# Kernel tuning notes

Hardware: AMD Instinct MI355X
Metric: run time of the kernel (lower is better)

Reference implementation:

```python
import jax, jax.numpy as jnp
import numpy as np

K = 20          # neighbors, hardcoded default in source
EPS = 1e-5      # BatchNorm2d default eps


def _knn(x, k=K):
    # x: (B, C, N). distance[b,i,j] = -||x_i - x_j||^2; top-k == first k of descending sort
    inner = -2.0 * jnp.einsum('bdn,bdm->bnm', x, x)
    xx = jnp.sum(x * x, axis=1)                      # (B, N)
    dist = -xx[:, :, None] - inner - xx[:, None, :]  # (B, N, N)
    return jax.lax.top_k(dist, k)[1]                 # (B, N, k) int32


def _graph_feature(x, k=K):
    idx = _knn(x, k)
    xt = jnp.transpose(x, (0, 2, 1))                 # (B, N, C)
    feat = jax.vmap(lambda a, i: a[i])(xt, idx)      # (B, N, k, C) gather
    center = jnp.broadcast_to(xt[:, :, None, :], feat.shape)
    out = jnp.concatenate([feat - center, center], axis=-1)  # (B, N, k, 2C)
    return jnp.transpose(out, (0, 3, 1, 2))          # (B, 2C, N, k)


def _conv_bn_relu(x, w, g, b):
    # 1x1 conv (no bias) + train-mode BatchNorm (batch stats) + ReLU
    y = jnp.einsum('oc,bcnk->bonk', w, x)
    m = jnp.mean(y, axis=(0, 2, 3), keepdims=True)
    v = jnp.var(y, axis=(0, 2, 3), keepdims=True)
    y = (y - m) * jax.lax.rsqrt(v + EPS)
    y = y * g[None, :, None, None] + b[None, :, None, None]
    return jax.nn.relu(y)


def setup_inputs() -> dict:
    key = jax.random.key(0)
    ks = jax.random.split(key, 8)
    B, C, N = 8, 3, 2048
    emb = 512
    x = jax.random.normal(ks[0], (B, C, N), dtype=jnp.float32)

    def w(k, o, i):
        return jax.random.normal(k, (o, i), dtype=jnp.float32) * np.sqrt(2.0 / i).astype(np.float32)

    d = {'x': x}
    dims = [(6, 64), (64, 64), (64, 128), (128, 256), (512, emb)]
    for n, (i, o) in enumerate(dims, start=1):
        d[f'w{n}'] = w(ks[n], o, i)
        d[f'g{n}'] = jnp.ones((o,), jnp.float32)
        d[f'b{n}'] = jnp.zeros((o,), jnp.float32)
    return d


def reference(x, w1, g1, b1, w2, g2, b2, w3, g3, b3, w4, g4, b4, w5, g5, b5):
    B, _, N = x.shape
    h = _graph_feature(x)                                  # (B, 6, N, k)
    h = _conv_bn_relu(h, w1, g1, b1); x1 = jnp.max(h, -1, keepdims=True)
    h = _conv_bn_relu(h, w2, g2, b2); x2 = jnp.max(h, -1, keepdims=True)
    h = _conv_bn_relu(h, w3, g3, b3); x3 = jnp.max(h, -1, keepdims=True)
    h = _conv_bn_relu(h, w4, g4, b4); x4 = jnp.max(h, -1, keepdims=True)
    o = jnp.concatenate([x1, x2, x3, x4], axis=1)          # (B, 512, N, 1)
    o = _conv_bn_relu(o, w5, g5, b5)                       # (B, 512, N, 1)
    return o.reshape(B, -1, N)
```

## Files before the change

### kernel.cpp

```cpp
#include <hip/hip_runtime.h>
#include <cstdint>
#include <cstddef>

#define BATCH 8
#define NPTS 2048
#define KNN 20
#define M1 327680
#define M2 16384

typedef unsigned short ushort_t;
typedef unsigned long long u64;
typedef __attribute__((ext_vector_type(8))) short bf16x8;
typedef __attribute__((ext_vector_type(4))) float f32x4;
typedef __attribute__((ext_vector_type(2))) int int2v;

#define OFF_XT    0UL
#define OFF_IDX   262144UL
#define OFF_WH2   1572864UL
#define OFF_WH3   1589248UL
#define OFF_WH4   1622016UL
#define OFF_WH5   1753088UL
#define OFF_SS    2842624UL
#define OFF_REG0  2863104UL
#define OFF_REG1  86749184UL
#define OFF_XCAT  128692224UL
#define OFF_RAWMAX 145469440UL
#define OFF_RAWMIN 162246656UL
#define OFF_SP     179023872UL
#define WS_NEEDED  181121024UL

__device__ __forceinline__ float bf2f(unsigned short u) {
    union { unsigned int i; float f; } c; c.i = ((unsigned int)u) << 16; return c.f;
}
__device__ __forceinline__ unsigned short f2bf(float f) {
    union { float f; unsigned int i; } c; c.f = f;
    unsigned int x = c.i;
    unsigned int r = (x + 0x7fffu + ((x >> 16) & 1u)) >> 16;
    return (unsigned short)r;
}
__device__ __forceinline__ unsigned int pack2(float a, float b) {
    return (unsigned int)f2bf(a) | ((unsigned int)f2bf(b) << 16);
}
__device__ __forceinline__ void unpack8(uint4 u, float* v) {
    v[0] = bf2f((unsigned short)(u.x & 0xffffu)); v[1] = bf2f((unsigned short)(u.x >> 16));
    v[2] = bf2f((unsigned short)(u.y & 0xffffu)); v[3] = bf2f((unsigned short)(u.y >> 16));
    v[4] = bf2f((unsigned short)(u.z & 0xffffu)); v[5] = bf2f((unsigned short)(u.z >> 16));
    v[6] = bf2f((unsigned short)(u.w & 0xffffu)); v[7] = bf2f((unsigned short)(u.w >> 16));
}

__global__ void prep_k(const float* __restrict__ x, float4* __restrict__ xt4) {
    int t = blockIdx.x * 256 + threadIdx.x;
    int b = t >> 11, n = t & 2047;
    float v0 = x[((size_t)b * 3 + 0) * NPTS + n];
    float v1 = x[((size_t)b * 3 + 1) * NPTS + n];
    float v2 = x[((size_t)b * 3 + 2) * NPTS + n];
    float xxv = __fadd_rn(__fadd_rn(__fmul_rn(v0, v0), __fmul_rn(v1, v1)), __fmul_rn(v2, v2));
    xt4[t] = make_float4(v0, v1, v2, xxv);
}

__global__ void wsplit_all_k(const float* __restrict__ w2, ushort_t* __restrict__ wh2,
                             const float* __restrict__ w3, ushort_t* __restrict__ wh3,
                             const float* __restrict__ w4, ushort_t* __restrict__ wh4,
                             const float* __restrict__ w5, ushort_t* __restrict__ wh5) {
    int t = blockIdx.x * 256 + threadIdx.x;
    if (t < 4096)        { wh2[t] = f2bf(w2[t]); }
    else if (t < 12288)  { int o = t - 4096;  wh3[o] = f2bf(w3[o]); }
    else if (t < 45056)  { int o = t - 12288; wh4[o] = f2bf(w4[o]); }
    else                 { int o = t - 45056; wh5[o] = f2bf(w5[o]); }
}


__device__ __forceinline__ unsigned okey(float f) {
    int u = __float_as_int(f);
    return (unsigned)(u ^ ((u >> 31) | 0x80000000));
}

#define DPP_ROR(x, n) __builtin_amdgcn_update_dpp(0, (x), 0x120 + (n), 0xf, 0xf, true)

template<int N>
__device__ __forceinline__ void ror_max(u64 &k) {
    unsigned h = (unsigned)DPP_ROR((int)(unsigned)(k >> 32), N);
    unsigned lo = (unsigned)DPP_ROR((int)(unsigned)k, N);
    u64 o = ((u64)h << 32) | lo;
    if (o > k) k = o;
}

__device__ __forceinline__ void swap16_max(u64 &k) {
    int2v ph = __builtin_amdgcn_permlane16_swap((int)(unsigned)(k >> 32), (int)(unsigned)(k >> 32), false, false);
    int2v pl = __builtin_amdgcn_permlane16_swap((int)(unsigned)k, (int)(unsigned)k, false, false);
    u64 a = ((u64)(unsigned)ph.x << 32) | (unsigned)pl.x;
    u64 b = ((u64)(unsigned)ph.y << 32) | (unsigned)pl.y;
    k = (b > a) ? b : a;
}

__device__ __forceinline__ void swap32_max(u64 &k) {
    int2v ph = __builtin_amdgcn_permlane32_swap((int)(unsigned)(k >> 32), (int)(unsigned)(k >> 32), false, false);
    int2v pl = __builtin_amdgcn_permlane32_swap((int)(unsigned)k, (int)(unsigned)k, false, false);
    u64 a = ((u64)(unsigned)ph.x << 32) | (unsigned)pl.x;
    u64 b = ((u64)(unsigned)ph.y << 32) | (unsigned)pl.y;
    k = (b > a) ? b : a;
}

template<int G>
__device__ __forceinline__ void knn_rescan(float (&v)[32], u64 (&gk)[4],
                                           bool own, int qw, unsigned laneC) {
#pragma unroll
    for (int q = G * 8; q < G * 8 + 8; q++)
        if (own && q == qw) v[q] = -3.4e38f;
    float m = v[G * 8]; int qi = G * 8;
#pragma unroll
    for (int q = G * 8 + 1; q < G * 8 + 8; q++)
        if (v[q] > m) { m = v[q]; qi = q; }
    gk[G] = ((u64)okey(m) << 32) | (laneC - (unsigned)(qi << 6));
}

__device__ __forceinline__ void knn_rescan_any(float (&v)[32], u64 (&gk)[4],
                                               int j, int l, unsigned laneC) {
    int qw = j >> 6;
    bool own = (l == (j & 63));
    int gw = qw >> 3;
    if (gw == 0)      knn_rescan<0>(v, gk, own, qw, laneC);
    else if (gw == 1) knn_rescan<1>(v, gk, own, qw, laneC);
    else if (gw == 2) knn_rescan<2>(v, gk, own, qw, laneC);
    else              knn_rescan<3>(v, gk, own, qw, laneC);
}

__launch_bounds__(256)
__global__ void knn_k(const float4* __restrict__ xt4, int* __restrict__ idx) {
    int tid = threadIdx.x;
    int l = tid & 63, wv = tid >> 6;
    int pidA = blockIdx.x * 8 + wv * 2;
    int pidB = pidA + 1;
    int b = pidA >> 11;
    const float4* xb4 = xt4 + (size_t)b * NPTS;
    int iA = pidA & 2047, iB = pidB & 2047;
    float4 PA = xb4[iA];
    float4 PB = xb4[iB];
    float vA[32], vB[32];
#pragma unroll
    for (int q = 0; q < 32; q++) {
        int j = l + q * 64;
        float4 p = xb4[j];
        float dA = __fadd_rn(__fadd_rn(__fmul_rn(PA.x, p.x), __fmul_rn(PA.y, p.y)), __fmul_rn(PA.z, p.z));
        float dB = __fadd_rn(__fadd_rn(__fmul_rn(PB.x, p.x), __fmul_rn(PB.y, p.y)), __fmul_rn(PB.z, p.z));
        vA[q] = __fsub_rn(__fsub_rn(-PA.w, __fmul_rn(-2.0f, dA)), p.w);
        vB[q] = __fsub_rn(__fsub_rn(-PB.w, __fmul_rn(-2.0f, dB)), p.w);
    }
    unsigned laneC = (unsigned)(2047 - l);
    u64 gkA[4], gkB[4];
#pragma unroll
    for (int g = 0; g < 4; g++) {
        float mA = vA[g * 8]; int qA = g * 8;
        float mB = vB[g * 8]; int qB = g * 8;
#pragma unroll
        for (int q = g * 8 + 1; q < g * 8 + 8; q++) {
            if (vA[q] > mA) { mA = vA[q]; qA = q; }
            if (vB[q] > mB) { mB = vB[q]; qB = q; }
        }
        gkA[g] = ((u64)okey(mA) << 32) | (laneC - (unsigned)(qA << 6));
        gkB[g] = ((u64)okey(mB) << 32) | (laneC - (unsigned)(qB << 6));
    }
    int* outA = idx + (size_t)pidA * KNN;
    int* outB = idx + (size_t)pidB * KNN;
    unsigned myj = 0;
#pragma unroll 1
    for (int t = 0; t < KNN; t++) {
        u64 kA = gkA[0], kB = gkB[0];
#pragma unroll
        for (int g = 1; g < 4; g++) {
            if (gkA[g] > kA) kA = gkA[g];
            if (gkB[g] > kB) kB = gkB[g];
        }
        ror_max<1>(kA); ror_max<1>(kB);
        ror_max<2>(kA); ror_max<2>(kB);
        ror_max<4>(kA); ror_max<4>(kB);
        ror_max<8>(kA); ror_max<8>(kB);
        swap16_max(kA); swap16_max(kB);
        swap32_max(kA); swap32_max(kB);
        unsigned jAv = 2047u - (unsigned)kA;
        unsigned jBv = 2047u - (unsigned)kB;
        myj = (l == t) ? jAv : myj;
        myj = (l == t + 32) ? jBv : myj;
        if (t == KNN - 1) break;
        int jA = 2047 - (int)(unsigned)__builtin_amdgcn_readfirstlane((int)(unsigned)kA);
        int jB = 2047 - (int)(unsigned)__builtin_amdgcn_readfirstlane((int)(unsigned)kB);
        knn_rescan_any(vA, gkA, jA, l, laneC);
        knn_rescan_any(vB, gkB, jB, l, laneC);
    }
    if (l < KNN) outA[l] = (int)myj;
    if (l >= 32 && l < 32 + KNN) outB[l - 32] = (int)myj;
}

__launch_bounds__(256, 2)
__global__ void conv1_fused_k(const float4* __restrict__ xt4, const int* __restrict__ idx,
                              const float* __restrict__ w1, ushort_t* __restrict__ y1,
                              float* __restrict__ rawmax, float* __restrict__ rawmin,
                              float* __restrict__ sp) {
    __shared__ ushort_t hA[320 * 56];
    __shared__ ushort_t wHs[64 * 56];
    __shared__ float sw[4 * 64 * 2];
    const int tid = threadIdx.x;
    const int m0 = blockIdx.x * 320;
    for (int i = tid; i < 512; i += 256) sw[i] = 0.0f;
    {
        int row = tid >> 2, seg = tid & 3;
        uint4 u = make_uint4(0, 0, 0, 0);
        if (seg == 0) {
            const float* wr = w1 + row * 6;
            u.x = pack2(wr[0], wr[1]);
            u.y = pack2(wr[2], wr[3]);
            u.z = pack2(wr[4], wr[5]);
        }
        *(uint4*)&wHs[row * 56 + seg * 8] = u;
    }
    for (int r = tid; r < 320; r += 256) {
        int m = m0 + r;
        int nb = m / KNN;
        int b = nb >> 11;
        int j = idx[m];
        float4 PI = xt4[nb];
        float4 PJ = xt4[(size_t)(b * NPTS + j)];
        uint4 u;
        u.x = pack2(PJ.x - PI.x, PJ.y - PI.y);
        u.y = pack2(PJ.z - PI.z, PI.x);
        u.z = pack2(PI.y, PI.z);
        u.w = 0;
        uint4 z = make_uint4(0, 0, 0, 0);
        *(uint4*)&hA[r * 56 + 0]  = u;
        *(uint4*)&hA[r * 56 + 8]  = z;
        *(uint4*)&hA[r * 56 + 16] = z;
        *(uint4*)&hA[r * 56 + 24] = z;
    }
    __syncthreads();
    const int lane = tid & 63, wv = tid >> 6;
    const int l15 = lane & 15, quad = lane >> 4;
    f32x4 acc[5][4];
#pragma unroll
    for (int mt = 0; mt < 5; mt++)
#pragma unroll
        for (int ot = 0; ot < 4; ot++) acc[mt][ot] = (f32x4){0.f, 0.f, 0.f, 0.f};
    bf16x8 a[5];
#pragma unroll
    for (int mt = 0; mt < 5; mt++)
        a[mt] = *(bf16x8*)&hA[(wv * 80 + mt * 16 + l15) * 56 + quad * 8];
#pragma unroll
    for (int ot = 0; ot < 4; ot++) {
        bf16x8 bh = *(bf16x8*)&wHs[(ot * 16 + l15) * 56 + quad * 8];
#pragma unroll
        for (int mt = 0; mt < 5; mt++)
            acc[mt][ot] = __builtin_amdgcn_mfma_f32_16x16x32_bf16(a[mt], bh, acc[mt][ot], 0, 0, 0);
    }
    __syncthreads();
    float* wreg = (float*)((char*)hA + wv * 6400);
#pragma unroll
    for (int ot = 0; ot < 4; ot++) {
#pragma unroll
        for (int mt = 0; mt < 5; mt++)
#pragma unroll
            for (int r = 0; r < 4; r++)
                wreg[(mt * 16 + quad * 4 + r) * 20 + l15] = acc[mt][ot][r];
        __syncthreads();
        {
            int pp = quad;
            const float* rr = wreg + (pp * 20) * 20 + l15;
            float mx = rr[0], mn = rr[0], sm = 0.0f, ss = 0.0f;
#pragma unroll
            for (int q = 0; q < 20; q++) {
                float vv = rr[q * 20];
                mx = fmaxf(mx, vv); mn = fminf(mn, vv);
                sm += vv; ss = fmaf(vv, vv, ss);
            }
            int pt = blockIdx.x * 16 + wv * 4 + pp;
            int o = ot * 16 + l15;
            rawmax[(size_t)pt * 64 + o] = mx;
            rawmin[(size_t)pt * 64 + o] = mn;
            sm += __shfl_xor(sm, 16); sm += __shfl_xor(sm, 32);
            ss += __shfl_xor(ss, 16); ss += __shfl_xor(ss, 32);
            if (lane < 16) {
                sw[(wv * 64 + ot * 16 + l15) * 2 + 0] += sm;
                sw[(wv * 64 + ot * 16 + l15) * 2 + 1] += ss;
            }
        }
#pragma unroll
        for (int it = 0; it < 3; it++) {
            int t = lane + it * 64;
            if (t < 160) {
                int row = t >> 1, half = t & 1;
                float4 f0 = *(float4*)&wreg[row * 20 + half * 8];
                float4 f1 = *(float4*)&wreg[row * 20 + half * 8 + 4];
                uint4 u;
                u.x = pack2(f0.x, f0.y); u.y = pack2(f0.z, f0.w);
                u.z = pack2(f1.x, f1.y); u.w = pack2(f1.z, f1.w);
                *(uint4*)(y1 + (size_t)(m0 + wv * 80 + row) * 64 + ot * 16 + half * 8) = u;
            }
        }
        __syncthreads();
    }
    if (tid < 128) {
        int ol = tid >> 1, st = tid & 1;
        float v = 0.0f;
#pragma unroll
        for (int w2 = 0; w2 < 4; w2++) v += sw[(w2 * 64 + ol) * 2 + st];
        sp[(size_t)blockIdx.x * 128 + ol * 2 + st] = v;
    }
}

template<int CIN, int COUT>
__launch_bounds__(256)
__global__ void conv5_mfma_k(const ushort_t* __restrict__ yin,
                             const ushort_t* __restrict__ whi,
                             ushort_t* __restrict__ yout,
                             float* __restrict__ sp) {
    __shared__ char smem[23552];
    ushort_t* hA = (ushort_t*)smem;
    ushort_t* wH = (ushort_t*)(smem + 14336);
    float* sw = (float*)(smem + 21504);
    const int tid = threadIdx.x;
    const int m0 = blockIdx.y * 128;
    const int o0 = blockIdx.x * 64;
    f32x4 acc[2][4];
#pragma unroll
    for (int mt = 0; mt < 2; mt++)
#pragma unroll
        for (int ot = 0; ot < 4; ot++) acc[mt][ot] = (f32x4){0.f, 0.f, 0.f, 0.f};
    const int lane = tid & 63, wv = tid >> 6;
    const int l15 = lane & 15, quad = lane >> 4;
    for (int kc = 0; kc < CIN; kc += 32) {
        __syncthreads();
#pragma unroll
        for (int i = 0; i < 2; i++) {
            int tt = tid + 256 * i;
            int mr = tt >> 2, cq = (tt & 3) * 8;
            *(uint4*)&hA[mr * 56 + cq] = *(const uint4*)(yin + (size_t)(m0 + mr) * CIN + kc + cq);
        }
        {
            int orow = tid >> 2, cq = (tid & 3) * 8;
            *(uint4*)&wH[orow * 56 + cq] = *(const uint4*)(whi + (size_t)(o0 + orow) * CIN + kc + cq);
        }
        __syncthreads();
        bf16x8 a0 = *(bf16x8*)&hA[(wv * 32 + l15) * 56 + quad * 8];
        bf16x8 a1 = *(bf16x8*)&hA[(wv * 32 + 16 + l15) * 56 + quad * 8];
#pragma unroll
        for (int ot = 0; ot < 4; ot++) {
            bf16x8 bh = *(bf16x8*)&wH[(ot * 16 + l15) * 56 + quad * 8];
            acc[0][ot] = __builtin_amdgcn_mfma_f32_16x16x32_bf16(a0, bh, acc[0][ot], 0, 0, 0);
            acc[1][ot] = __builtin_amdgcn_mfma_f32_16x16x32_bf16(a1, bh, acc[1][ot], 0, 0, 0);
        }
    }
#pragma unroll
    for (int ot = 0; ot < 4; ot++) {
        float sm = 0.0f, ss = 0.0f;
#pragma unroll
        for (int mt = 0; mt < 2; mt++)
#pragma unroll
            for (int r = 0; r < 4; r++) {
                float v = acc[mt][ot][r];
                sm += v; ss = fmaf(v, v, ss);
            }
        sm += __shfl_xor(sm, 16); sm += __shfl_xor(sm, 32);
        ss += __shfl_xor(ss, 16); ss += __shfl_xor(ss, 32);
        if (lane < 16) {
            sw[(wv * 64 + ot * 16 + l15) * 2 + 0] = sm;
            sw[(wv * 64 + ot * 16 + l15) * 2 + 1] = ss;
        }
    }
    __syncthreads();
    ushort_t* outT = (ushort_t*)smem;
#pragma unroll
    for (int mt = 0; mt < 2; mt++)
#pragma unroll
        for (int ot = 0; ot < 4; ot++)
#pragma unroll
            for (int r = 0; r < 4; r++)
                outT[(wv * 32 + mt * 16 + quad * 4 + r) * 72 + ot * 16 + l15] = f2bf(acc[mt][ot][r]);
    __syncthreads();
    int row = tid >> 1, half = tid & 1;
#pragma unroll
    for (int g = 0; g < 4; g++) {
        uint4 u = *(uint4*)&outT[row * 72 + half * 32 + g * 8];
        *(uint4*)(yout + (size_t)(m0 + row) * COUT + o0 + half * 32 + g * 8) = u;
    }
    if (tid < 128) {
        int ol = tid >> 1, st = tid & 1;
        float v = 0.0f;
#pragma unroll
        for (int w2 = 0; w2 < 4; w2++) v += sw[(w2 * 64 + ol) * 2 + st];
        size_t bid = (size_t)blockIdx.x * gridDim.y + blockIdx.y;
        sp[bid * 128 + ol * 2 + st] = v;
    }
}

template<int CIN, int COUT, int BO, bool WRITEY>
__launch_bounds__(256, 2)
__global__ void conv_fused_k(const ushort_t* __restrict__ yin,
                             const ushort_t* __restrict__ whi,
                             const float* __restrict__ scale,
                             const float* __restrict__ shift,
                             ushort_t* __restrict__ yout,
                             float* __restrict__ rawmax, float* __restrict__ rawmin,
                             float* __restrict__ sp) {
    constexpr int NOT = BO / 16;
    __shared__ ushort_t hA[320 * 56];
    __shared__ ushort_t wHs[BO * 56];
    __shared__ float scl[CIN], shf[CIN];
    __shared__ float sw[4 * BO * 2];
    const int tid = threadIdx.x;
    const int m0 = blockIdx.y * 320;
    const int o0 = blockIdx.x * BO;
    for (int c = tid; c < CIN; c += 256) { scl[c] = scale[c]; shf[c] = shift[c]; }
    for (int i = tid; i < 4 * BO * 2; i += 256) sw[i] = 0.0f;
    f32x4 acc[5][NOT];
#pragma unroll
    for (int mt = 0; mt < 5; mt++)
#pragma unroll
        for (int ot = 0; ot < NOT; ot++) acc[mt][ot] = (f32x4){0.f, 0.f, 0.f, 0.f};
    const int lane = tid & 63, wv = tid >> 6;
    const int l15 = lane & 15, quad = lane >> 4;
    for (int kc = 0; kc < CIN; kc += 32) {
        __syncthreads();
#pragma unroll
        for (int i = 0; i < 5; i++) {
            int tt = tid + 256 * i;
            int mr = tt >> 2, cq = (tt & 3) * 8;
            uint4 u = *(const uint4*)(yin + (size_t)(m0 + mr) * CIN + kc + cq);
            float vv[8]; unpack8(u, vv);
#pragma unroll
            for (int e = 0; e < 8; e++)
                vv[e] = fmaxf(fmaf(vv[e], scl[kc + cq + e], shf[kc + cq + e]), 0.0f);
            u.x = pack2(vv[0], vv[1]); u.y = pack2(vv[2], vv[3]);
            u.z = pack2(vv[4], vv[5]); u.w = pack2(vv[6], vv[7]);
            *(uint4*)&hA[mr * 56 + cq] = u;
        }
        for (int t = tid; t < BO * 4; t += 256) {
            int row = t >> 2, cq = (t & 3) * 8;
            *(uint4*)&wHs[row * 56 + cq] = *(const uint4*)(whi + (size_t)(o0 + row) * CIN + kc + cq);
        }
        __syncthreads();
        bf16x8 a[5];
#pragma unroll
        for (int mt = 0; mt < 5; mt++)
            a[mt] = *(bf16x8*)&hA[(wv * 80 + mt * 16 + l15) * 56 + quad * 8];
#pragma unroll
        for (int ot = 0; ot < NOT; ot++) {
            bf16x8 bh = *(bf16x8*)&wHs[(ot * 16 + l15) * 56 + quad * 8];
#pragma unroll
            for (int mt = 0; mt < 5; mt++)
                acc[mt][ot] = __builtin_amdgcn_mfma_f32_16x16x32_bf16(a[mt], bh, acc[mt][ot], 0, 0, 0);
        }
    }
    __syncthreads();
    float* wreg = (float*)((char*)hA + wv * 6400);
#pragma unroll
    for (int ot = 0; ot < NOT; ot++) {
#pragma unroll
        for (int mt = 0; mt < 5; mt++)
#pragma unroll
            for (int r = 0; r < 4; r++)
                wreg[(mt * 16 + quad * 4 + r) * 20 + l15] = acc[mt][ot][r];
        __syncthreads();
        {
            int pp = quad;
            const float* rr = wreg + (pp * 20) * 20 + l15;
            float mx = rr[0], mn = rr[0], sm = 0.0f, ss = 0.0f;
#pragma unroll
            for (int q = 0; q < 20; q++) {
                float vv = rr[q * 20];
                mx = fmaxf(mx, vv); mn = fminf(mn, vv);
                sm += vv; ss = fmaf(vv, vv, ss);
            }
            int pt = blockIdx.y * 16 + wv * 4 + pp;
            int o = o0 + ot * 16 + l15;
            rawmax[(size_t)pt * COUT + o] = mx;
            rawmin[(size_t)pt * COUT + o] = mn;
            sm += __shfl_xor(sm, 16); sm += __shfl_xor(sm, 32);
            ss += __shfl_xor(ss, 16); ss += __shfl_xor(ss, 32);
            if (lane < 16) {
                sw[(wv * BO + ot * 16 + l15) * 2 + 0] += sm;
                sw[(wv * BO + ot * 16 + l15) * 2 + 1] += ss;
            }
        }
        if constexpr (WRITEY) {
#pragma unroll
            for (int it = 0; it < 3; it++) {
                int t = lane + it * 64;
                if (t < 160) {
                    int row = t >> 1, half = t & 1;
                    float4 f0 = *(float4*)&wreg[row * 20 + half * 8];
                    float4 f1 = *(float4*)&wreg[row * 20 + half * 8 + 4];
                    uint4 u;
                    u.x = pack2(f0.x, f0.y); u.y = pack2(f0.z, f0.w);
                    u.z = pack2(f1.x, f1.y); u.w = pack2(f1.z, f1.w);
                    *(uint4*)(yout + (size_t)(m0 + wv * 80 + row) * COUT + o0 + ot * 16 + half * 8) = u;
                }
            }
        }
        __syncthreads();
    }
    for (int t2 = tid; t2 < BO * 2; t2 += 256) {
        int ol = t2 >> 1, st = t2 & 1;
        float v = 0.0f;
#pragma unroll
        for (int w2 = 0; w2 < 4; w2++) v += sw[(w2 * BO + ol) * 2 + st];
        size_t bid = (size_t)blockIdx.x * 1024 + blockIdx.y;
        sp[bid * (2 * BO) + ol * 2 + st] = v;
    }
}

template<int BO, int MB>
__launch_bounds__(256)
__global__ void statsred_fin_k(const float* __restrict__ sp,
                               const float* __restrict__ g, const float* __restrict__ bb,
                               float* __restrict__ scale, float* __restrict__ shift,
                               double invcnt) {
    __shared__ double rs[256], rss[256];
    int o = blockIdx.x, tid = threadIdx.x;
    int oy = o / BO, ol = o % BO;
    double s = 0.0, ss = 0.0;
    for (int mb = tid; mb < MB; mb += 256) {
        size_t bid = (size_t)oy * MB + mb;
        s  += (double)sp[bid * (2 * BO) + ol * 2 + 0];
        ss += (double)sp[bid * (2 * BO) + ol * 2 + 1];
    }
    rs[tid] = s; rss[tid] = ss;
    __syncthreads();
    for (int st = 128; st; st >>= 1) {
        if (tid < st) { rs[tid] += rs[tid + st]; rss[tid] += rss[tid + st]; }
        __syncthreads();
    }
    if (tid == 0) {
        double m = rs[0] * invcnt;
        double v = rss[0] * invcnt - m * m;
        if (v < 0.0) v = 0.0;
        float sc = g[o] / sqrtf((float)v + 1e-5f);
        scale[o] = sc;
        shift[o] = bb[o] - (float)m * sc;
    }
}

template<int C8>
__launch_bounds__(256)
__global__ void pool_raw_k(const float* __restrict__ rawmax, const float* __restrict__ rawmin,
                           const float* __restrict__ scale, const float* __restrict__ shift,
                           ushort_t* __restrict__ xcat, int coff) {
    constexpr int COUT = C8 * 8;
    int gid = blockIdx.x * 256 + threadIdx.x;
    int p = gid / C8, og = gid % C8;
    float sc[8], sh[8], mxv[8], mnv[8];
    *(float4*)&sc[0]  = *(const float4*)(scale + og * 8);
    *(float4*)&sc[4]  = *(const float4*)(scale + og * 8 + 4);
    *(float4*)&sh[0]  = *(const float4*)(shift + og * 8);
    *(float4*)&sh[4]  = *(const float4*)(shift + og * 8 + 4);
    *(float4*)&mxv[0] = *(const float4*)(rawmax + (size_t)p * COUT + og * 8);
    *(float4*)&mxv[4] = *(const float4*)(rawmax + (size_t)p * COUT + og * 8 + 4);
    *(float4*)&mnv[0] = *(const float4*)(rawmin + (size_t)p * COUT + og * 8);
    *(float4*)&mnv[4] = *(const float4*)(rawmin + (size_t)p * COUT + og * 8 + 4);
    float v[8];
#pragma unroll
    for (int e = 0; e < 8; e++) {
        float raw = (sc[e] >= 0.0f) ? mxv[e] : mnv[e];
        v[e] = fmaxf(fmaf(raw, sc[e], sh[e]), 0.0f);
    }
    uint4 u;
    u.x = pack2(v[0], v[1]); u.y = pack2(v[2], v[3]);
    u.z = pack2(v[4], v[5]); u.w = pack2(v[6], v[7]);
    *(uint4*)(xcat + (size_t)p * 512 + coff + og * 8) = u;
}

__launch_bounds__(256)
__global__ void out_k(const ushort_t* __restrict__ y5, const float* __restrict__ scale,
                      const float* __restrict__ shift, float* __restrict__ out) {
    __shared__ float tr[64 * 65];
    int tid = threadIdx.x;
    int n0 = blockIdx.x * 64, c0 = blockIdx.y * 64, b = blockIdx.z;
    int nl = tid >> 2, cq = (tid & 3) * 16;
    const ushort_t* src = y5 + (size_t)(b * 2048 + n0 + nl) * 512 + c0 + cq;
#pragma unroll
    for (int h = 0; h < 2; h++) {
        uint4 u = *(const uint4*)(src + h * 8);
        float vv[8]; unpack8(u, vv);
#pragma unroll
        for (int e = 0; e < 8; e++) {
            int c = cq + h * 8 + e;
            tr[c * 65 + nl] = fmaxf(fmaf(vv[e], scale[c0 + c], shift[c0 + c]), 0.0f);
        }
    }
    __syncthreads();
    int cl = tid >> 2, ng = (tid & 3) * 16;
#pragma unroll
    for (int g = 0; g < 4; g++) {
        float4 v = *(float4*)&tr[cl * 65 + ng + g * 4];
        *(float4*)(out + ((size_t)b * 512 + c0 + cl) * 2048 + n0 + ng + g * 4) = v;
    }
}

extern "C" void kernel_launch(void* const* d_in, const int* in_sizes, int n_in,
                              void* d_out, int out_size, void* d_ws, size_t ws_size,
                              hipStream_t stream) {
    (void)in_sizes; (void)n_in; (void)out_size;
    if (ws_size < WS_NEEDED) return;
    const float* x  = (const float*)d_in[0];
    const float* w1 = (const float*)d_in[1];
    const float* g1 = (const float*)d_in[2];
    const float* b1 = (const float*)d_in[3];
    const float* w2 = (const float*)d_in[4];
    const float* g2 = (const float*)d_in[5];
    const float* b2 = (const float*)d_in[6];
    const float* w3 = (const float*)d_in[7];
    const float* g3 = (const float*)d_in[8];
    const float* b3 = (const float*)d_in[9];
    const float* w4 = (const float*)d_in[10];
    const float* g4 = (const float*)d_in[11];
    const float* b4 = (const float*)d_in[12];
    const float* w5 = (const float*)d_in[13];
    const float* g5 = (const float*)d_in[14];
    const float* b5 = (const float*)d_in[15];

    char* ws = (char*)d_ws;
    float4* xt4 = (float4*)(ws + OFF_XT);
    int*   idx = (int*)(ws + OFF_IDX);
    ushort_t* wh2 = (ushort_t*)(ws + OFF_WH2);
    ushort_t* wh3 = (ushort_t*)(ws + OFF_WH3);
    ushort_t* wh4 = (ushort_t*)(ws + OFF_WH4);
    ushort_t* wh5 = (ushort_t*)(ws + OFF_WH5);
    ushort_t* y1 = (ushort_t*)(ws + OFF_REG0);
    ushort_t* y2 = (ushort_t*)(ws + OFF_REG1);
    ushort_t* y3 = (ushort_t*)(ws + OFF_REG0);
    ushort_t* y5 = (ushort_t*)(ws + OFF_REG0);
    ushort_t* xcat = (ushort_t*)(ws + OFF_XCAT);
    float* rawmax = (float*)(ws + OFF_RAWMAX);
    float* rawmin = (float*)(ws + OFF_RAWMIN);
    float* sp     = (float*)(ws + OFF_SP);

    float* scl[5]; float* shf[5];
    for (int l = 0; l < 5; l++) {
        scl[l] = (float*)(ws + OFF_SS + (size_t)l * 4096);
        shf[l] = scl[l] + 512;
    }

    prep_k<<<64, 256, 0, stream>>>(x, xt4);
    wsplit_all_k<<<1200, 256, 0, stream>>>(w2, wh2, w3, wh3, w4, wh4, w5, wh5);
    knn_k<<<2048, 256, 0, stream>>>(xt4, idx);

    conv1_fused_k<<<1024, 256, 0, stream>>>(xt4, idx, w1, y1, rawmax, rawmin, sp);
    statsred_fin_k<64, 1024><<<64, 256, 0, stream>>>(sp, g1, b1, scl[0], shf[0], 1.0 / 327680.0);
    pool_raw_k<8><<<512, 256, 0, stream>>>(rawmax, rawmin, scl[0], shf[0], xcat, 0);

    conv_fused_k<64, 64, 64, true><<<dim3(1, 1024), 256, 0, stream>>>(
        y1, wh2, scl[0], shf[0], y2, rawmax, rawmin, sp);
    statsred_fin_k<64, 1024><<<64, 256, 0, stream>>>(sp, g2, b2, scl[1], shf[1], 1.0 / 327680.0);
    pool_raw_k<8><<<512, 256, 0, stream>>>(rawmax, rawmin, scl[1], shf[1], xcat, 64);

    conv_fused_k<64, 128, 128, true><<<dim3(1, 1024), 256, 0, stream>>>(
        y2, wh3, scl[1], shf[1], y3, rawmax, rawmin, sp);
    statsred_fin_k<128, 1024><<<128, 256, 0, stream>>>(sp, g3, b3, scl[2], shf[2], 1.0 / 327680.0);
    pool_raw_k<16><<<1024, 256, 0, stream>>>(rawmax, rawmin, scl[2], shf[2], xcat, 128);

    conv_fused_k<128, 256, 128, false><<<dim3(2, 1024), 256, 0, stream>>>(
        y3, wh4, scl[2], shf[2], nullptr, rawmax, rawmin, sp);
    statsred_fin_k<128, 1024><<<256, 256, 0, stream>>>(sp, g4, b4, scl[3], shf[3], 1.0 / 327680.0);
    pool_raw_k<32><<<2048, 256, 0, stream>>>(rawmax, rawmin, scl[3], shf[3], xcat, 256);

    conv5_mfma_k<512, 512><<<dim3(8, 128), 256, 0, stream>>>(xcat, wh5, y5, sp);
    statsred_fin_k<64, 128><<<512, 256, 0, stream>>>(sp, g5, b5, scl[4], shf[4], 1.0 / 16384.0);
    out_k<<<dim3(32, 8, 8), 256, 0, stream>>>(y5, scl[4], shf[4], (float*)d_out);
}
```

Measured before the change: 436.3 us.

## Split kNN wavefront into two half-waves and use fp64 max keys

The kNN kernel now gives each query point its own 32-lane half of the wavefront, with 64 candidates per lane, instead of having all 64 lanes handle two queries. The cross-lane argmax reduction drops the 32-lane swap stage and does one reduction chain for both queries. Keys are packed into a positive double so a single fmax replaces the 64-bit integer compare. This costs more registers per lane (64 distances, 8 group keys) and makes the rescan branch divergent between the two halves.

```diff
diff --git a/kernel.cpp b/kernel.cpp
--- a/kernel.cpp
+++ b/kernel.cpp
@@ -70,40 +70,36 @@
 }
 
 
-__device__ __forceinline__ unsigned okey(float f) {
-    int u = __float_as_int(f);
-    return (unsigned)(u ^ ((u >> 31) | 0x80000000));
+__device__ __forceinline__ double mkkey(float m, unsigned idx11) {
+    int u = __float_as_int(m);
+    unsigned ok = (unsigned)(u ^ ((u >> 31) | 0x80000000));
+    u64 k = (1ull << 62) | ((u64)ok << 30) | (u64)idx11;
+    return __longlong_as_double((long long)k);
 }
 
 #define DPP_ROR(x, n) __builtin_amdgcn_update_dpp(0, (x), 0x120 + (n), 0xf, 0xf, true)
 
 template<int N>
-__device__ __forceinline__ void ror_max(u64 &k) {
-    unsigned h = (unsigned)DPP_ROR((int)(unsigned)(k >> 32), N);
-    unsigned lo = (unsigned)DPP_ROR((int)(unsigned)k, N);
-    u64 o = ((u64)h << 32) | lo;
-    if (o > k) k = o;
-}
-
-__device__ __forceinline__ void swap16_max(u64 &k) {
-    int2v ph = __builtin_amdgcn_permlane16_swap((int)(unsigned)(k >> 32), (int)(unsigned)(k >> 32), false, false);
-    int2v pl = __builtin_amdgcn_permlane16_swap((int)(unsigned)k, (int)(unsigned)k, false, false);
-    u64 a = ((u64)(unsigned)ph.x << 32) | (unsigned)pl.x;
-    u64 b = ((u64)(unsigned)ph.y << 32) | (unsigned)pl.y;
-    k = (b > a) ? b : a;
-}
-
-__device__ __forceinline__ void swap32_max(u64 &k) {
-    int2v ph = __builtin_amdgcn_permlane32_swap((int)(unsigned)(k >> 32), (int)(unsigned)(k >> 32), false, false);
-    int2v pl = __builtin_amdgcn_permlane32_swap((int)(unsigned)k, (int)(unsigned)k, false, false);
-    u64 a = ((u64)(unsigned)ph.x << 32) | (unsigned)pl.x;
-    u64 b = ((u64)(unsigned)ph.y << 32) | (unsigned)pl.y;
-    k = (b > a) ? b : a;
+__device__ __forceinline__ void ror_max(double &k) {
+    u64 u = (u64)__double_as_longlong(k);
+    unsigned h  = (unsigned)DPP_ROR((int)(unsigned)(u >> 32), N);
+    unsigned lo = (unsigned)DPP_ROR((int)(unsigned)u, N);
+    double o = __longlong_as_double((long long)(((u64)h << 32) | lo));
+    k = fmax(k, o);
+}
+
+__device__ __forceinline__ void swap16_max(double &k) {
+    u64 u = (u64)__double_as_longlong(k);
+    int2v ph = __builtin_amdgcn_permlane16_swap((int)(unsigned)(u >> 32), (int)(unsigned)(u >> 32), false, false);
+    int2v pl = __builtin_amdgcn_permlane16_swap((int)(unsigned)u, (int)(unsigned)u, false, false);
+    double a = __longlong_as_double((long long)(((u64)(unsigned)ph.x << 32) | (unsigned)pl.x));
+    double b = __longlong_as_double((long long)(((u64)(unsigned)ph.y << 32) | (unsigned)pl.y));
+    k = fmax(a, b);
 }
 
 template<int G>
-__device__ __forceinline__ void knn_rescan(float (&v)[32], u64 (&gk)[4],
-                                           bool own, int qw, unsigned laneC) {
+__device__ __forceinline__ void knn_rescan8(float (&v)[64], double (&gk)[8],
+                                            bool own, int qw, int lane31) {
 #pragma unroll
     for (int q = G * 8; q < G * 8 + 8; q++)
         if (own && q == qw) v[q] = -3.4e38f;
@@ -111,84 +107,72 @@
 #pragma unroll
     for (int q = G * 8 + 1; q < G * 8 + 8; q++)
         if (v[q] > m) { m = v[q]; qi = q; }
-    gk[G] = ((u64)okey(m) << 32) | (laneC - (unsigned)(qi << 6));
-}
-
-__device__ __forceinline__ void knn_rescan_any(float (&v)[32], u64 (&gk)[4],
-                                               int j, int l, unsigned laneC) {
-    int qw = j >> 6;
-    bool own = (l == (j & 63));
-    int gw = qw >> 3;
-    if (gw == 0)      knn_rescan<0>(v, gk, own, qw, laneC);
-    else if (gw == 1) knn_rescan<1>(v, gk, own, qw, laneC);
-    else if (gw == 2) knn_rescan<2>(v, gk, own, qw, laneC);
-    else              knn_rescan<3>(v, gk, own, qw, laneC);
+    gk[G] = mkkey(m, 2047u - (unsigned)(lane31 + (qi << 5)));
+}
+
+__device__ __forceinline__ void knn_rescan_any8(float (&v)[64], double (&gk)[8],
+                                                int j, int lane31) {
+    int qw = j >> 5;
+    bool own = (lane31 == (j & 31));
+    switch (qw >> 3) {
+        case 0: knn_rescan8<0>(v, gk, own, qw, lane31); break;
+        case 1: knn_rescan8<1>(v, gk, own, qw, lane31); break;
+        case 2: knn_rescan8<2>(v, gk, own, qw, lane31); break;
+        case 3: knn_rescan8<3>(v, gk, own, qw, lane31); break;
+        case 4: knn_rescan8<4>(v, gk, own, qw, lane31); break;
+        case 5: knn_rescan8<5>(v, gk, own, qw, lane31); break;
+        case 6: knn_rescan8<6>(v, gk, own, qw, lane31); break;
+        default: knn_rescan8<7>(v, gk, own, qw, lane31); break;
+    }
 }
 
 __launch_bounds__(256)
 __global__ void knn_k(const float4* __restrict__ xt4, int* __restrict__ idx) {
     int tid = threadIdx.x;
     int l = tid & 63, wv = tid >> 6;
-    int pidA = blockIdx.x * 8 + wv * 2;
-    int pidB = pidA + 1;
-    int b = pidA >> 11;
+    int lane31 = l & 31, half = l >> 5;
+    int basePid = blockIdx.x * 8 + wv * 2;
+    int pid = basePid + half;
+    int b = pid >> 11;
     const float4* xb4 = xt4 + (size_t)b * NPTS;
-    int iA = pidA & 2047, iB = pidB & 2047;
-    float4 PA = xb4[iA];
-    float4 PB = xb4[iB];
-    float vA[32], vB[32];
-#pragma unroll
-    for (int q = 0; q < 32; q++) {
-        int j = l + q * 64;
-        float4 p = xb4[j];
-        float dA = __fadd_rn(__fadd_rn(__fmul_rn(PA.x, p.x), __fmul_rn(PA.y, p.y)), __fmul_rn(PA.z, p.z));
-        float dB = __fadd_rn(__fadd_rn(__fmul_rn(PB.x, p.x), __fmul_rn(PB.y, p.y)), __fmul_rn(PB.z, p.z));
-        vA[q] = __fsub_rn(__fsub_rn(-PA.w, __fmul_rn(-2.0f, dA)), p.w);
-        vB[q] = __fsub_rn(__fsub_rn(-PB.w, __fmul_rn(-2.0f, dB)), p.w);
-    }
-    unsigned laneC = (unsigned)(2047 - l);
-    u64 gkA[4], gkB[4];
-#pragma unroll
-    for (int g = 0; g < 4; g++) {
-        float mA = vA[g * 8]; int qA = g * 8;
-        float mB = vB[g * 8]; int qB = g * 8;
-#pragma unroll
-        for (int q = g * 8 + 1; q < g * 8 + 8; q++) {
-            if (vA[q] > mA) { mA = vA[q]; qA = q; }
-            if (vB[q] > mB) { mB = vB[q]; qB = q; }
-        }
-        gkA[g] = ((u64)okey(mA) << 32) | (laneC - (unsigned)(qA << 6));
-        gkB[g] = ((u64)okey(mB) << 32) | (laneC - (unsigned)(qB << 6));
-    }
-    int* outA = idx + (size_t)pidA * KNN;
-    int* outB = idx + (size_t)pidB * KNN;
+    float4 P = xb4[pid & 2047];
+    float v[64];
+#pragma unroll
+    for (int q = 0; q < 64; q++) {
+        float4 p = xb4[lane31 + q * 32];
+        float d = __fadd_rn(__fadd_rn(__fmul_rn(P.x, p.x), __fmul_rn(P.y, p.y)), __fmul_rn(P.z, p.z));
+        v[q] = __fsub_rn(__fsub_rn(-P.w, __fmul_rn(-2.0f, d)), p.w);
+    }
+    double gk[8];
+#pragma unroll
+    for (int g = 0; g < 8; g++) {
+        float m = v[g * 8]; int qi = g * 8;
+#pragma unroll
+        for (int q = g * 8 + 1; q < g * 8 + 8; q++)
+            if (v[q] > m) { m = v[q]; qi = q; }
+        gk[g] = mkkey(m, 2047u - (unsigned)(lane31 + (qi << 5)));
+    }
     unsigned myj = 0;
 #pragma unroll 1
     for (int t = 0; t < KNN; t++) {
-        u64 kA = gkA[0], kB = gkB[0];
-#pragma unroll
-        for (int g = 1; g < 4; g++) {
-            if (gkA[g] > kA) kA = gkA[g];
-            if (gkB[g] > kB) kB = gkB[g];
-        }
-        ror_max<1>(kA); ror_max<1>(kB);
-        ror_max<2>(kA); ror_max<2>(kB);
-        ror_max<4>(kA); ror_max<4>(kB);
-        ror_max<8>(kA); ror_max<8>(kB);
-        swap16_max(kA); swap16_max(kB);
-        swap32_max(kA); swap32_max(kB);
-        unsigned jAv = 2047u - (unsigned)kA;
-        unsigned jBv = 2047u - (unsigned)kB;
-        myj = (l == t) ? jAv : myj;
-        myj = (l == t + 32) ? jBv : myj;
+        double k = fmax(fmax(fmax(gk[0], gk[1]), fmax(gk[2], gk[3])),
+                        fmax(fmax(gk[4], gk[5]), fmax(gk[6], gk[7])));
+        ror_max<1>(k); ror_max<2>(k); ror_max<4>(k); ror_max<8>(k);
+        swap16_max(k);
+        unsigned lo = (unsigned)(u64)__double_as_longlong(k);
+        unsigned jv = 2047u - (lo & 2047u);
+        myj = (l == t) ? jv : myj;
+        myj = (l == t + 32) ? jv : myj;
         if (t == KNN - 1) break;
-        int jA = 2047 - (int)(unsigned)__builtin_amdgcn_readfirstlane((int)(unsigned)kA);
-        int jB = 2047 - (int)(unsigned)__builtin_amdgcn_readfirstlane((int)(unsigned)kB);
-        knn_rescan_any(vA, gkA, jA, l, laneC);
-        knn_rescan_any(vB, gkB, jB, l, laneC);
-    }
-    if (l < KNN) outA[l] = (int)myj;
-    if (l >= 32 && l < 32 + KNN) outB[l - 32] = (int)myj;
+        int loA = __builtin_amdgcn_readlane((int)lo, 0);
+        int loB = __builtin_amdgcn_readlane((int)lo, 32);
+        int jA = 2047 - (loA & 2047);
+        int jB = 2047 - (loB & 2047);
+        if (l < 32) knn_rescan_any8(v, gk, jA, lane31);
+        else        knn_rescan_any8(v, gk, jB, lane31);
+    }
+    if (l < KNN) idx[(size_t)basePid * KNN + l] = (int)myj;
+    else if (l >= 32 && l < 32 + KNN) idx[(size_t)(basePid + 1) * KNN + (l - 32)] = (int)myj;
 }
 
 __launch_bounds__(256, 2)
```

New measurement: 504.6 us. +15.7%, slower.
